# Optimization experiments

Measured on AMD Instinct MI355X. Metric: run time of the kernel, lower is better.

## Reference

```python
import jax, jax.numpy as jnp
import numpy as np

B = 65536
N_SPARSE = 26
N_DENSE = 13
EMB = 5
VOCAB = 100000
N_EXPERTS = 4
D_IN = N_DENSE + N_SPARSE * EMB  # 143
H1, H2 = 128, 64


def setup_inputs() -> dict:
    key = jax.random.key(0)
    ks = jax.random.split(key, 16)
    s = 0.05
    return {
        "sparse_inputs": jax.random.randint(ks[0], (B, N_SPARSE), 0, VOCAB),
        "dense_inputs": jax.random.normal(ks[1], (B, N_DENSE), dtype=jnp.float32),
        "emb_tables": jax.random.normal(ks[2], (N_SPARSE, VOCAB, EMB), dtype=jnp.float32) * s,
        "expert_W1": jax.random.normal(ks[3], (N_EXPERTS, D_IN, H1), dtype=jnp.float32) * s,
        "expert_b1": jnp.zeros((N_EXPERTS, H1), dtype=jnp.float32),
        "expert_W2": jax.random.normal(ks[4], (N_EXPERTS, H1, H2), dtype=jnp.float32) * s,
        "expert_b2": jnp.zeros((N_EXPERTS, H2), dtype=jnp.float32),
        "gate_finish_W": jax.random.normal(ks[5], (D_IN, N_EXPERTS), dtype=jnp.float32) * s,
        "gate_finish_b": jnp.zeros((N_EXPERTS,), dtype=jnp.float32),
        "gate_like_W": jax.random.normal(ks[6], (D_IN, N_EXPERTS), dtype=jnp.float32) * s,
        "gate_like_b": jnp.zeros((N_EXPERTS,), dtype=jnp.float32),
        "finish_W": jax.random.normal(ks[7], (H2, 1), dtype=jnp.float32) * s,
        "finish_b": jnp.zeros((1,), dtype=jnp.float32),
        "like_W": jax.random.normal(ks[8], (H2, 1), dtype=jnp.float32) * s,
        "like_b": jnp.zeros((1,), dtype=jnp.float32),
    }


def reference(sparse_inputs, dense_inputs, emb_tables, expert_W1, expert_b1,
              expert_W2, expert_b2, gate_finish_W, gate_finish_b,
              gate_like_W, gate_like_b, finish_W, finish_b, like_W, like_b):
    # per-feature embedding lookup: [B, N_SPARSE, EMB]
    feat_idx = jnp.arange(N_SPARSE)[None, :]
    sp_emb = emb_tables[feat_idx, sparse_inputs]
    x = jnp.concatenate([dense_inputs, sp_emb.reshape(sparse_inputs.shape[0], -1)], axis=1)  # [B, D_IN]

    # batched expert MLPs (dropout is inactive at inference)
    h = jax.nn.relu(jnp.einsum('bd,edh->beh', x, expert_W1) + expert_b1)  # [B, E, 128]
    expert_out = jax.nn.relu(jnp.einsum('beh,eho->beo', h, expert_W2) + expert_b2)  # [B, E, 64]

    gate_f = jax.nn.softmax(x @ gate_finish_W + gate_finish_b, axis=-1)  # [B, E]
    gate_l = jax.nn.softmax(x @ gate_like_W + gate_like_b, axis=-1)

    task_finish = jnp.einsum('be,beo->bo', gate_f, expert_out)  # [B, 64]
    task_like = jnp.einsum('be,beo->bo', gate_l, expert_out)

    finish = jax.nn.sigmoid(task_finish @ finish_W + finish_b)  # [B, 1]
    like = jax.nn.sigmoid(task_like @ like_W + like_b)  # [B, 1]
    return finish, like
```

## Files before the change

### kernel.cpp

```cpp
#include <hip/hip_runtime.h>
#include <math.h>

#define NB     65536
#define NSP    26
#define NDN    13
#define EMBD   5
#define VOCAB  100000
#define NE     4
#define DIN    143
#define KPAD   160
#define H1     128
#define H2     64

typedef __attribute__((ext_vector_type(8))) short bf16x8;
typedef __attribute__((ext_vector_type(4))) float f32x4;

__device__ __forceinline__ unsigned short f2bf(float f) {
    unsigned int u = __float_as_uint(f);
    u = (u + 0x7fff + ((u >> 16) & 1)) >> 16;
    return (unsigned short)u;
}

__device__ __forceinline__ unsigned cvtpk(float lo, float hi) {
    unsigned r;
    asm("v_cvt_pk_bf16_f32 %0, %1, %2" : "=v"(r) : "v"(lo), "v"(hi));
    return r;
}

__device__ __forceinline__ void gll16(const unsigned short* g, unsigned short* l) {
    __builtin_amdgcn_global_load_lds(
        (const __attribute__((address_space(1))) unsigned int*)g,
        (__attribute__((address_space(3))) unsigned int*)l, 16, 0, 0);
}

#define E1 (4*8*5*512)
#define E2 (4*4*4*512)
#define E3 (5*512)
#define NWE (E1+E2+E3)
#define GBLKS 1024
#define PBLKS ((NWE+255)/256)


__global__ __launch_bounds__(256)
void gather_pack(const int*   __restrict__ sparse,
                 const float* __restrict__ dense,
                 const float* __restrict__ emb,
                 const float* __restrict__ W1,  const float* __restrict__ W2,
                 const float* __restrict__ gfW, const float* __restrict__ glW,
                 unsigned short* __restrict__ w1p, unsigned short* __restrict__ w2p,
                 unsigned short* __restrict__ gwp, unsigned short* __restrict__ xg)
{
    const int blk = blockIdx.x;
    const int tid = threadIdx.x;
    if (blk < GBLKS) {
        __shared__ int idxs[64 * NSP];
        __shared__ __align__(16) unsigned short xs[64][168];
        const int row0 = blk * 64;

        for (int t = tid; t < 64 * NSP; t += 256)
            idxs[t] = sparse[row0 * NSP + t];
        for (int t = tid; t < 64 * NDN; t += 256) {
            int r = t / NDN, c = t - r * NDN;
            xs[r][c] = f2bf(dense[(row0 + r) * NDN + c]);
        }
        for (int t = tid; t < 64 * (KPAD - DIN); t += 256) {
            int r = t / (KPAD - DIN), c = DIN + (t - r * (KPAD - DIN));
            xs[r][c] = 0;
        }
        __syncthreads();
        for (int t = tid; t < 64 * NSP * EMBD; t += 256) {
            int f = t / (64 * EMBD);
            int rem = t - f * (64 * EMBD);
            int r = rem / EMBD, c = rem - r * EMBD;
            int idx = idxs[r * NSP + f];
            float v = emb[((size_t)f * VOCAB + idx) * EMBD + c];
            xs[r][NDN + f * EMBD + c] = f2bf(v);
        }
        __syncthreads();
        for (int v = tid; v < 4 * 5 * 64; v += 256) {
            int lo = v & 63, chunk = v >> 6;
            int s = chunk % 5, tl = chunk / 5;
            int b = lo & 15, g = lo >> 4;
            bf16x8 val = *(const bf16x8*)&xs[tl * 16 + b][32 * s + 8 * g];
            *(bf16x8*)(xg + ((size_t)((blk * 4 + tl) * 5 + s) * 64 + lo) * 8) = val;
        }
        return;
    }

    int i = (blk - GBLKS) * 256 + tid;
    if (i < E1) {
        int j = i & 7, l = (i >> 3) & 63;
        int rest = i >> 9;
        int s = rest % 5; rest /= 5;
        int nt = rest & 7, e = rest >> 3;
        int b = l & 15, g = l >> 4;
        int k = 32 * s + 8 * g + j;
        int n = nt * 16 + b;
        w1p[i] = (k < DIN) ? f2bf(W1[(e * DIN + k) * H1 + n]) : (unsigned short)0;
        return;
    }
    i -= E1;
    if (i < E2) {
        int j = i & 7, l = (i >> 3) & 63;
        int rest = i >> 9;
        int s = rest & 3; rest >>= 2;
        int ot = rest & 3, e = rest >> 2;
        int b = l & 15, g = l >> 4;
        int k = 32 * s + 8 * g + j;
        int o = ot * 16 + b;
        w2p[i] = f2bf(W2[(e * H1 + k) * H2 + o]);
        return;
    }
    i -= E2;
    if (i < E3) {
        int j = i & 7, l = (i >> 3) & 63;
        int s = i >> 9;
        int b = l & 15, g = l >> 4;
        int k = 32 * s + 8 * g + j;
        float v = 0.f;
        if (k < DIN) {
            if (b < 4)      v = gfW[k * NE + b];
            else if (b < 8) v = glW[k * NE + (b - 4)];
        }
        gwp[i] = f2bf(v);
    }
}

__global__ __launch_bounds__(512, 4)
void mmoe10(const unsigned short* __restrict__ xg,
            const unsigned short* __restrict__ w1p, const float* __restrict__ b1,
            const unsigned short* __restrict__ w2p, const float* __restrict__ b2,
            const unsigned short* __restrict__ gwp,
            const float* __restrict__ gfb, const float* __restrict__ glb,
            const float* __restrict__ fW,  const float* __restrict__ lW,
            float* __restrict__ acc)
{
    __shared__ __align__(16) unsigned short wlds[28672];
    __shared__ __align__(16) char hsb[16384];

    const int tid  = threadIdx.x;
    const int wid  = tid >> 6;
    const int lane = tid & 63;
    const int b    = lane & 15;
    const int g    = lane >> 4;
    const int q    = blockIdx.x >> 5;
    const int r5   = blockIdx.x & 31;
    const int e    = r5 >> 3;
    const int rg   = q * 8 + (r5 & 7);
    const int t0   = rg * 8 + wid;
    const int swz  = (b & 7) << 4;
    char* const hw = hsb + wid * 2048 + b * 128;

    #pragma unroll
    for (int i = 0; i < 7; ++i) {
        int c = wid * 7 + i;
        if (c < 40)
            gll16(w1p + (((size_t)e * 40 + c) * 64 + lane) * 8, wlds + c * 512);
        else
            gll16(w2p + (((size_t)e * 16 + (c - 40)) * 64 + lane) * 8,
                  wlds + 20480 + (c - 40) * 512);
    }

    bf16x8 xf[5];
    #pragma unroll
    for (int s = 0; s < 5; ++s)
        xf[s] = *(const bf16x8*)(xg + ((size_t)(t0 * 5 + s) * 64 + lane) * 8);

    f32x4 ga = {0.f, 0.f, 0.f, 0.f};
    #pragma unroll
    for (int s = 0; s < 5; ++s) {
        bf16x8 af = *(const bf16x8*)(gwp + (size_t)(s * 64 + lane) * 8);
        ga = __builtin_amdgcn_mfma_f32_16x16x32_bf16(af, xf[s], ga, 0, 0, 0);
    }
    const float4 gfb4 = *(const float4*)gfb;
    const float4 glb4 = *(const float4*)glb;
    float gfv, glv;
    {
        const float4 bias = (g == 1) ? glb4 : gfb4;
        float l0 = ga[0] + bias.x, l1 = ga[1] + bias.y;
        float l2 = ga[2] + bias.z, l3 = ga[3] + bias.w;
        float m = fmaxf(fmaxf(l0, l1), fmaxf(l2, l3));
        float e0 = expf(l0 - m), e1 = expf(l1 - m), e2 = expf(l2 - m), e3 = expf(l3 - m);
        float inv = 1.f / (e0 + e1 + e2 + e3);
        float sel = (e == 0) ? e0 : (e == 1) ? e1 : (e == 2) ? e2 : e3;
        sel *= inv;
        gfv = __shfl(sel, b);
        glv = __shfl(sel, b + 16);
    }

    __syncthreads();

    f32x4 c[4];
    #pragma unroll
    for (int ot = 0; ot < 4; ++ot) c[ot] = (f32x4){0.f, 0.f, 0.f, 0.f};

    #pragma unroll
    for (int h = 0; h < 2; ++h) {
        #pragma unroll
        for (int nl = 0; nl < 4; ++nl) {
            const int nt = h * 4 + nl;
            bf16x8 wv[5];
            #pragma unroll
            for (int s = 0; s < 5; ++s)
                wv[s] = *(const bf16x8*)(wlds + ((nt * 5 + s) * 64 + lane) * 8);
            f32x4 a2 = {0.f, 0.f, 0.f, 0.f};
            #pragma unroll
            for (int s = 0; s < 5; ++s)
                a2 = __builtin_amdgcn_mfma_f32_16x16x32_bf16(wv[s], xf[s], a2, 0, 0, 0);
            const float4 b1v = *(const float4*)(b1 + e * H1 + nt * 16 + 4 * g);
            uint2 hv;
            hv.x = cvtpk(fmaxf(a2[0] + b1v.x, 0.f), fmaxf(a2[1] + b1v.y, 0.f));
            hv.y = cvtpk(fmaxf(a2[2] + b1v.z, 0.f), fmaxf(a2[3] + b1v.w, 0.f));
            *(uint2*)(hw + ((nl * 32 + g * 8) ^ swz)) = hv;
        }
        bf16x8 hf[2];
        #pragma unroll
        for (int sl = 0; sl < 2; ++sl)
            hf[sl] = *(const bf16x8*)(hw + ((sl * 64 + g * 16) ^ swz));
        #pragma unroll
        for (int ot = 0; ot < 4; ++ot) {
            #pragma unroll
            for (int sl = 0; sl < 2; ++sl) {
                bf16x8 wv2 = *(const bf16x8*)(wlds + 20480 + ((ot * 4 + 2 * h + sl) * 64 + lane) * 8);
                c[ot] = __builtin_amdgcn_mfma_f32_16x16x32_bf16(wv2, hf[sl], c[ot], 0, 0, 0);
            }
        }
    }

    float vf = 0.f, vl = 0.f;
    #pragma unroll
    for (int ot = 0; ot < 4; ++ot) {
        const float4 b2v = *(const float4*)(b2 + e * H2 + ot * 16 + 4 * g);
        const float4 fwv = *(const float4*)(fW + ot * 16 + 4 * g);
        const float4 lwv = *(const float4*)(lW + ot * 16 + 4 * g);
        float o0 = fmaxf(c[ot][0] + b2v.x, 0.f), o1 = fmaxf(c[ot][1] + b2v.y, 0.f);
        float o2 = fmaxf(c[ot][2] + b2v.z, 0.f), o3 = fmaxf(c[ot][3] + b2v.w, 0.f);
        vf += gfv * (o0 * fwv.x + o1 * fwv.y + o2 * fwv.z + o3 * fwv.w);
        vl += glv * (o0 * lwv.x + o1 * lwv.y + o2 * lwv.z + o3 * lwv.w);
    }

    vf += __shfl_xor(vf, 16); vf += __shfl_xor(vf, 32);
    vl += __shfl_xor(vl, 16); vl += __shfl_xor(vl, 32);
    if (g == 0) {
        int r = t0 * 16 + b;
        acc[(size_t)e * NB + r]       = vf;
        acc[(size_t)(4 + e) * NB + r] = vl;
    }
}

__global__ __launch_bounds__(256)
void heads_ep(const float* __restrict__ acc,
              const float* __restrict__ fb, const float* __restrict__ lb,
              float* __restrict__ out)
{
    int r = blockIdx.x * 256 + threadIdx.x;
    float sf = acc[r] + acc[NB + r] + acc[2 * NB + r] + acc[3 * NB + r];
    float sl = acc[4 * NB + r] + acc[5 * NB + r] + acc[6 * NB + r] + acc[7 * NB + r];
    out[r]      = 1.f / (1.f + expf(-(sf + fb[0])));
    out[NB + r] = 1.f / (1.f + expf(-(sl + lb[0])));
}


__global__ __launch_bounds__(256)
void preproc(const float* __restrict__ W1, const float* __restrict__ W2,
             const float* __restrict__ gfW, const float* __restrict__ glW,
             unsigned short* __restrict__ w1t, unsigned short* __restrict__ w2t,
             unsigned short* __restrict__ gwc)
{
    int i = blockIdx.x * 256 + threadIdx.x;
    if (i < 4*128*160) {
        int k = i % KPAD;
        int n = (i / KPAD) & (H1 - 1);
        int e = i / (KPAD * H1);
        w1t[i] = (k < DIN) ? f2bf(W1[(e * DIN + k) * H1 + n]) : (unsigned short)0;
    } else if (i < 4*128*160 + 4*64*128) {
        int j = i - 4*128*160;
        int k = j & (H1 - 1);
        int o = (j >> 7) & (H2 - 1);
        int e = j >> 13;
        w2t[j] = f2bf(W2[(e * H1 + k) * H2 + o]);
    } else if (i < 4*128*160 + 4*64*128 + 16*160) {
        int j = i - (4*128*160 + 4*64*128);
        int k = j % KPAD;
        int r = j / KPAD;
        float v = 0.f;
        if (k < DIN) {
            if (r < 4)      v = gfW[k * NE + r];
            else if (r < 8) v = glW[k * NE + (r - 4)];
        }
        gwc[j] = f2bf(v);
    }
}

__global__ __launch_bounds__(256)
void mmoe_mfma(const int*   __restrict__ sparse,
               const float* __restrict__ dense,
               const float* __restrict__ emb,
               const unsigned short* __restrict__ w1t,
               const float* __restrict__ b1,
               const unsigned short* __restrict__ w2t,
               const float* __restrict__ b2,
               const unsigned short* __restrict__ gwc,
               const float* __restrict__ gfb, const float* __restrict__ glb,
               const float* __restrict__ fW,  const float* __restrict__ fb,
               const float* __restrict__ lW,  const float* __restrict__ lb,
               float* __restrict__ out)
{
    __shared__ __align__(16) unsigned short xs[64][KPAD];
    __shared__ __align__(16) unsigned short hs[64][136];
    __shared__ __align__(16) float gts[64][8];

    const int tid   = threadIdx.x;
    const int wid   = tid >> 6;
    const int lane  = tid & 63;
    const int b     = lane & 15;
    const int g     = lane >> 4;
    const int rbase = wid * 16;
    const int grow0 = blockIdx.x * 64 + rbase;

    for (int t = lane; t < 16 * NDN; t += 64) {
        int r = t & 15, d = t >> 4;
        xs[rbase + r][d] = f2bf(dense[(grow0 + r) * NDN + d]);
    }
    for (int t = lane; t < 16 * (KPAD - DIN); t += 64) {
        int r = t & 15, d = DIN + (t >> 4);
        xs[rbase + r][d] = 0;
    }
    for (int t = lane; t < 16 * NSP; t += 64) {
        int r = t & 15, f = t >> 4;
        int idx = sparse[(grow0 + r) * NSP + f];
        const float* ep = emb + (f * VOCAB + idx) * EMBD;
        int c0 = NDN + EMBD * f;
        #pragma unroll
        for (int c = 0; c < EMBD; ++c)
            xs[rbase + r][c0 + c] = f2bf(ep[c]);
    }

    bf16x8 xf[5];
    #pragma unroll
    for (int s = 0; s < 5; ++s)
        xf[s] = *(const bf16x8*)&xs[rbase + b][32 * s + 8 * g];

    f32x4 ga = {0.f, 0.f, 0.f, 0.f};
    #pragma unroll
    for (int s = 0; s < 5; ++s) {
        bf16x8 af = *(const bf16x8*)(gwc + b * KPAD + 32 * s + 8 * g);
        ga = __builtin_amdgcn_mfma_f32_16x16x32_bf16(af, xf[s], ga, 0, 0, 0);
    }
    if (g < 2) {
        const float4 bias = *(const float4*)(g ? glb : gfb);
        float l0 = ga[0] + bias.x, l1 = ga[1] + bias.y;
        float l2 = ga[2] + bias.z, l3 = ga[3] + bias.w;
        float m = fmaxf(fmaxf(l0, l1), fmaxf(l2, l3));
        float e0 = expf(l0 - m), e1 = expf(l1 - m), e2 = expf(l2 - m), e3 = expf(l3 - m);
        float inv = 1.f / (e0 + e1 + e2 + e3);
        float4 gv; gv.x = e0 * inv; gv.y = e1 * inv; gv.z = e2 * inv; gv.w = e3 * inv;
        *(float4*)&gts[rbase + b][g * 4] = gv;
    }

    float vf = 0.f, vl = 0.f;
    for (int e = 0; e < NE; ++e) {
        const unsigned short* w1e = w1t + e * (H1 * KPAD);
        #pragma unroll
        for (int nt = 0; nt < 8; ++nt) {
            f32x4 acc = {0.f, 0.f, 0.f, 0.f};
            #pragma unroll
            for (int s = 0; s < 5; ++s) {
                bf16x8 af = *(const bf16x8*)(w1e + (nt * 16 + b) * KPAD + 32 * s + 8 * g);
                acc = __builtin_amdgcn_mfma_f32_16x16x32_bf16(af, xf[s], acc, 0, 0, 0);
            }
            const float4 b1v = *(const float4*)(b1 + e * H1 + nt * 16 + 4 * g);
            unsigned lo = (unsigned)f2bf(fmaxf(acc[0] + b1v.x, 0.f)) |
                          ((unsigned)f2bf(fmaxf(acc[1] + b1v.y, 0.f)) << 16);
            unsigned hi = (unsigned)f2bf(fmaxf(acc[2] + b1v.z, 0.f)) |
                          ((unsigned)f2bf(fmaxf(acc[3] + b1v.w, 0.f)) << 16);
            uint2 hv; hv.x = lo; hv.y = hi;
            *(uint2*)&hs[rbase + b][nt * 16 + 4 * g] = hv;
        }

        bf16x8 hf[4];
        #pragma unroll
        for (int s = 0; s < 4; ++s)
            hf[s] = *(const bf16x8*)&hs[rbase + b][32 * s + 8 * g];

        float gf = gts[rbase + b][e];
        float gl = gts[rbase + b][4 + e];
        const unsigned short* w2e = w2t + e * (H2 * H1);
        #pragma unroll
        for (int ot = 0; ot < 4; ++ot) {
            f32x4 acc = {0.f, 0.f, 0.f, 0.f};
            #pragma unroll
            for (int s = 0; s < 4; ++s) {
                bf16x8 af = *(const bf16x8*)(w2e + (ot * 16 + b) * H1 + 32 * s + 8 * g);
                acc = __builtin_amdgcn_mfma_f32_16x16x32_bf16(af, hf[s], acc, 0, 0, 0);
            }
            const float4 b2v = *(const float4*)(b2 + e * H2 + ot * 16 + 4 * g);
            const float4 fwv = *(const float4*)(fW + ot * 16 + 4 * g);
            const float4 lwv = *(const float4*)(lW + ot * 16 + 4 * g);
            float o0 = fmaxf(acc[0] + b2v.x, 0.f);
            float o1 = fmaxf(acc[1] + b2v.y, 0.f);
            float o2 = fmaxf(acc[2] + b2v.z, 0.f);
            float o3 = fmaxf(acc[3] + b2v.w, 0.f);
            vf += gf * (o0 * fwv.x + o1 * fwv.y + o2 * fwv.z + o3 * fwv.w);
            vl += gl * (o0 * lwv.x + o1 * lwv.y + o2 * lwv.z + o3 * lwv.w);
        }
    }

    vf += __shfl_xor(vf, 16); vf += __shfl_xor(vf, 32);
    vl += __shfl_xor(vl, 16); vl += __shfl_xor(vl, 32);
    if (g == 0) {
        int r = grow0 + b;
        out[r]      = 1.f / (1.f + expf(-(vf + fb[0])));
        out[NB + r] = 1.f / (1.f + expf(-(vl + lb[0])));
    }
}


extern "C" void kernel_launch(void* const* d_in, const int* in_sizes, int n_in,
                              void* d_out, int out_size, void* d_ws, size_t ws_size,
                              hipStream_t stream) {
    const int*   sparse = (const int*)  d_in[0];
    const float* dense  = (const float*)d_in[1];
    const float* emb    = (const float*)d_in[2];
    const float* W1     = (const float*)d_in[3];
    const float* b1     = (const float*)d_in[4];
    const float* W2     = (const float*)d_in[5];
    const float* b2     = (const float*)d_in[6];
    const float* gfW    = (const float*)d_in[7];
    const float* gfb    = (const float*)d_in[8];
    const float* glW    = (const float*)d_in[9];
    const float* glb    = (const float*)d_in[10];
    const float* fW     = (const float*)d_in[11];
    const float* fb     = (const float*)d_in[12];
    const float* lW     = (const float*)d_in[13];
    const float* lb     = (const float*)d_in[14];

    const size_t XG_BYTES  = (size_t)NB * KPAD * 2;
    const size_t W_BYTES   = (size_t)NWE * 2;
    const size_t ACC_BYTES = (size_t)2 * 4 * NB * 4;
    const size_t NEED = XG_BYTES + W_BYTES + ACC_BYTES;

    if (ws_size >= NEED) {
        unsigned short* xg  = (unsigned short*)d_ws;
        unsigned short* w1p = (unsigned short*)((char*)d_ws + XG_BYTES);
        unsigned short* w2p = (unsigned short*)((char*)d_ws + XG_BYTES + (size_t)E1 * 2);
        unsigned short* gwp = (unsigned short*)((char*)d_ws + XG_BYTES + (size_t)(E1 + E2) * 2);
        float*          acc = (float*)((char*)d_ws + XG_BYTES + W_BYTES);

        gather_pack<<<GBLKS + PBLKS, 256, 0, stream>>>(
            sparse, dense, emb, W1, W2, gfW, glW, w1p, w2p, gwp, xg);
        mmoe10<<<2048, 512, 0, stream>>>(xg, w1p, b1, w2p, b2, gwp,
                                         gfb, glb, fW, lW, acc);
        heads_ep<<<NB / 256, 256, 0, stream>>>(acc, fb, lb, (float*)d_out);
    } else {
        unsigned short* w1t = (unsigned short*)d_ws;
        unsigned short* w2t = (unsigned short*)((char*)d_ws + 163840);
        unsigned short* gwc = (unsigned short*)((char*)d_ws + 229376);

        int tot = 4*128*160 + 4*64*128 + 16*160;
        preproc<<<(tot + 255) / 256, 256, 0, stream>>>(W1, W2, gfW, glW, w1t, w2t, gwc);
        mmoe_mfma<<<NB / 64, 256, 0, stream>>>(sparse, dense, emb,
                                               w1t, b1, w2t, b2, gwc,
                                               gfb, glb, fW, fb, lW, lb,
                                               (float*)d_out);
    }
}
```

Measured before the change: 63.45 us.

## Fuse gather and heads into single MMoE kernel looping over experts per block

Moves the embedding gather into the main kernel, which builds the bf16 input tile in shared memory instead of reading a staged xg buffer. Each block now loops over all four experts, reloading that expert's packed weights into shared memory each time, and applies the sigmoid heads directly. This removes the xg round trip through global memory, the acc partial-sum buffer and the heads_ep launch. In exchange, weights are reloaded four times per block behind syncthreads with no overlap, and occupancy drops to 256-thread blocks using 64KB of shared memory.

Result: slower. 77.19 us (+21.7%).

```diff
diff --git a/kernel.cpp b/kernel.cpp
--- a/kernel.cpp
+++ b/kernel.cpp
@@ -37,57 +37,16 @@
 #define E2 (4*4*4*512)
 #define E3 (5*512)
 #define NWE (E1+E2+E3)
-#define GBLKS 1024
 #define PBLKS ((NWE+255)/256)
 
 
 __global__ __launch_bounds__(256)
-void gather_pack(const int*   __restrict__ sparse,
-                 const float* __restrict__ dense,
-                 const float* __restrict__ emb,
-                 const float* __restrict__ W1,  const float* __restrict__ W2,
+void weight_pack(const float* __restrict__ W1,  const float* __restrict__ W2,
                  const float* __restrict__ gfW, const float* __restrict__ glW,
                  unsigned short* __restrict__ w1p, unsigned short* __restrict__ w2p,
-                 unsigned short* __restrict__ gwp, unsigned short* __restrict__ xg)
+                 unsigned short* __restrict__ gwp)
 {
-    const int blk = blockIdx.x;
-    const int tid = threadIdx.x;
-    if (blk < GBLKS) {
-        __shared__ int idxs[64 * NSP];
-        __shared__ __align__(16) unsigned short xs[64][168];
-        const int row0 = blk * 64;
-
-        for (int t = tid; t < 64 * NSP; t += 256)
-            idxs[t] = sparse[row0 * NSP + t];
-        for (int t = tid; t < 64 * NDN; t += 256) {
-            int r = t / NDN, c = t - r * NDN;
-            xs[r][c] = f2bf(dense[(row0 + r) * NDN + c]);
-        }
-        for (int t = tid; t < 64 * (KPAD - DIN); t += 256) {
-            int r = t / (KPAD - DIN), c = DIN + (t - r * (KPAD - DIN));
-            xs[r][c] = 0;
-        }
-        __syncthreads();
-        for (int t = tid; t < 64 * NSP * EMBD; t += 256) {
-            int f = t / (64 * EMBD);
-            int rem = t - f * (64 * EMBD);
-            int r = rem / EMBD, c = rem - r * EMBD;
-            int idx = idxs[r * NSP + f];
-            float v = emb[((size_t)f * VOCAB + idx) * EMBD + c];
-            xs[r][NDN + f * EMBD + c] = f2bf(v);
-        }
-        __syncthreads();
-        for (int v = tid; v < 4 * 5 * 64; v += 256) {
-            int lo = v & 63, chunk = v >> 6;
-            int s = chunk % 5, tl = chunk / 5;
-            int b = lo & 15, g = lo >> 4;
-            bf16x8 val = *(const bf16x8*)&xs[tl * 16 + b][32 * s + 8 * g];
-            *(bf16x8*)(xg + ((size_t)((blk * 4 + tl) * 5 + s) * 64 + lo) * 8) = val;
-        }
-        return;
-    }
-
-    int i = (blk - GBLKS) * 256 + tid;
+    int i = blockIdx.x * 256 + threadIdx.x;
     if (i < E1) {
         int j = i & 7, l = (i >> 3) & 63;
         int rest = i >> 9;
@@ -126,45 +85,57 @@
     }
 }
 
-__global__ __launch_bounds__(512, 4)
-void mmoe10(const unsigned short* __restrict__ xg,
+__global__ __launch_bounds__(256, 2)
+void mmoe11(const int*   __restrict__ sparse,
+            const float* __restrict__ dense,
+            const float* __restrict__ emb,
             const unsigned short* __restrict__ w1p, const float* __restrict__ b1,
             const unsigned short* __restrict__ w2p, const float* __restrict__ b2,
             const unsigned short* __restrict__ gwp,
             const float* __restrict__ gfb, const float* __restrict__ glb,
-            const float* __restrict__ fW,  const float* __restrict__ lW,
-            float* __restrict__ acc)
+            const float* __restrict__ fW,  const float* __restrict__ fb,
+            const float* __restrict__ lW,  const float* __restrict__ lb,
+            float* __restrict__ out)
 {
-    __shared__ __align__(16) unsigned short wlds[28672];
-    __shared__ __align__(16) char hsb[16384];
+    __shared__ __align__(16) char uni[65536];
+    unsigned short* const xs   = (unsigned short*)uni;
+    int*            const idxs = (int*)(uni + 21504);
+    unsigned short* const wlds = (unsigned short*)uni;
+    char*           const hsb  = uni + 57344;
 
     const int tid  = threadIdx.x;
     const int wid  = tid >> 6;
     const int lane = tid & 63;
     const int b    = lane & 15;
     const int g    = lane >> 4;
-    const int q    = blockIdx.x >> 5;
-    const int r5   = blockIdx.x & 31;
-    const int e    = r5 >> 3;
-    const int rg   = q * 8 + (r5 & 7);
-    const int t0   = rg * 8 + wid;
+    const int row0 = blockIdx.x * 64;
     const int swz  = (b & 7) << 4;
     char* const hw = hsb + wid * 2048 + b * 128;
 
-    #pragma unroll
-    for (int i = 0; i < 7; ++i) {
-        int c = wid * 7 + i;
-        if (c < 40)
-            gll16(w1p + (((size_t)e * 40 + c) * 64 + lane) * 8, wlds + c * 512);
-        else
-            gll16(w2p + (((size_t)e * 16 + (c - 40)) * 64 + lane) * 8,
-                  wlds + 20480 + (c - 40) * 512);
-    }
+    for (int t = tid; t < 64 * NSP; t += 256)
+        idxs[t] = sparse[row0 * NSP + t];
+    for (int t = tid; t < 64 * NDN; t += 256) {
+        int r = t / NDN, c = t - r * NDN;
+        xs[r * 168 + c] = f2bf(dense[(row0 + r) * NDN + c]);
+    }
+    for (int t = tid; t < 64 * (KPAD - DIN); t += 256) {
+        int r = t / 17, c = DIN + (t - r * 17);
+        xs[r * 168 + c] = 0;
+    }
+    __syncthreads();
+    for (int t = tid; t < 64 * NSP * EMBD; t += 256) {
+        int f = t / 320;
+        int rem = t - f * 320;
+        int r = rem / EMBD, c = rem - r * EMBD;
+        int idx = idxs[r * NSP + f];
+        xs[r * 168 + NDN + f * EMBD + c] = f2bf(emb[((size_t)f * VOCAB + idx) * EMBD + c]);
+    }
+    __syncthreads();
 
     bf16x8 xf[5];
     #pragma unroll
     for (int s = 0; s < 5; ++s)
-        xf[s] = *(const bf16x8*)(xg + ((size_t)(t0 * 5 + s) * 64 + lane) * 8);
+        xf[s] = *(const bf16x8*)&xs[(wid * 16 + b) * 168 + 32 * s + 8 * g];
 
     f32x4 ga = {0.f, 0.f, 0.f, 0.f};
     #pragma unroll
@@ -172,92 +143,93 @@
         bf16x8 af = *(const bf16x8*)(gwp + (size_t)(s * 64 + lane) * 8);
         ga = __builtin_amdgcn_mfma_f32_16x16x32_bf16(af, xf[s], ga, 0, 0, 0);
     }
-    const float4 gfb4 = *(const float4*)gfb;
-    const float4 glb4 = *(const float4*)glb;
-    float gfv, glv;
+    f32x4 gn;
     {
-        const float4 bias = (g == 1) ? glb4 : gfb4;
+        const float4 bias = (g == 1) ? *(const float4*)glb : *(const float4*)gfb;
         float l0 = ga[0] + bias.x, l1 = ga[1] + bias.y;
         float l2 = ga[2] + bias.z, l3 = ga[3] + bias.w;
         float m = fmaxf(fmaxf(l0, l1), fmaxf(l2, l3));
         float e0 = expf(l0 - m), e1 = expf(l1 - m), e2 = expf(l2 - m), e3 = expf(l3 - m);
         float inv = 1.f / (e0 + e1 + e2 + e3);
-        float sel = (e == 0) ? e0 : (e == 1) ? e1 : (e == 2) ? e2 : e3;
-        sel *= inv;
-        gfv = __shfl(sel, b);
-        glv = __shfl(sel, b + 16);
+        gn[0] = e0 * inv; gn[1] = e1 * inv; gn[2] = e2 * inv; gn[3] = e3 * inv;
     }
 
     __syncthreads();
-
-    f32x4 c[4];
-    #pragma unroll
-    for (int ot = 0; ot < 4; ++ot) c[ot] = (f32x4){0.f, 0.f, 0.f, 0.f};
-
-    #pragma unroll
-    for (int h = 0; h < 2; ++h) {
-        #pragma unroll
-        for (int nl = 0; nl < 4; ++nl) {
-            const int nt = h * 4 + nl;
-            bf16x8 wv[5];
-            #pragma unroll
-            for (int s = 0; s < 5; ++s)
-                wv[s] = *(const bf16x8*)(wlds + ((nt * 5 + s) * 64 + lane) * 8);
-            f32x4 a2 = {0.f, 0.f, 0.f, 0.f};
-            #pragma unroll
-            for (int s = 0; s < 5; ++s)
-                a2 = __builtin_amdgcn_mfma_f32_16x16x32_bf16(wv[s], xf[s], a2, 0, 0, 0);
-            const float4 b1v = *(const float4*)(b1 + e * H1 + nt * 16 + 4 * g);
-            uint2 hv;
-            hv.x = cvtpk(fmaxf(a2[0] + b1v.x, 0.f), fmaxf(a2[1] + b1v.y, 0.f));
-            hv.y = cvtpk(fmaxf(a2[2] + b1v.z, 0.f), fmaxf(a2[3] + b1v.w, 0.f));
-            *(uint2*)(hw + ((nl * 32 + g * 8) ^ swz)) = hv;
-        }
-        bf16x8 hf[2];
-        #pragma unroll
-        for (int sl = 0; sl < 2; ++sl)
-            hf[sl] = *(const bf16x8*)(hw + ((sl * 64 + g * 16) ^ swz));
-        #pragma unroll
-        for (int ot = 0; ot < 4; ++ot) {
-            #pragma unroll
-            for (int sl = 0; sl < 2; ++sl) {
-                bf16x8 wv2 = *(const bf16x8*)(wlds + 20480 + ((ot * 4 + 2 * h + sl) * 64 + lane) * 8);
-                c[ot] = __builtin_amdgcn_mfma_f32_16x16x32_bf16(wv2, hf[sl], c[ot], 0, 0, 0);
-            }
-        }
-    }
 
     float vf = 0.f, vl = 0.f;
     #pragma unroll
-    for (int ot = 0; ot < 4; ++ot) {
-        const float4 b2v = *(const float4*)(b2 + e * H2 + ot * 16 + 4 * g);
-        const float4 fwv = *(const float4*)(fW + ot * 16 + 4 * g);
-        const float4 lwv = *(const float4*)(lW + ot * 16 + 4 * g);
-        float o0 = fmaxf(c[ot][0] + b2v.x, 0.f), o1 = fmaxf(c[ot][1] + b2v.y, 0.f);
-        float o2 = fmaxf(c[ot][2] + b2v.z, 0.f), o3 = fmaxf(c[ot][3] + b2v.w, 0.f);
-        vf += gfv * (o0 * fwv.x + o1 * fwv.y + o2 * fwv.z + o3 * fwv.w);
-        vl += glv * (o0 * lwv.x + o1 * lwv.y + o2 * lwv.z + o3 * lwv.w);
+    for (int e = 0; e < NE; ++e) {
+        if (e > 0) __syncthreads();
+        #pragma unroll
+        for (int i = 0; i < 14; ++i) {
+            int c = wid * 14 + i;
+            if (c < 40)
+                gll16(w1p + (((size_t)e * 40 + c) * 64 + lane) * 8, wlds + c * 512);
+            else
+                gll16(w2p + (((size_t)e * 16 + (c - 40)) * 64 + lane) * 8,
+                      wlds + 20480 + (c - 40) * 512);
+        }
+        __syncthreads();
+
+        const float gfv = __shfl(gn[e], b);
+        const float glv = __shfl(gn[e], b + 16);
+
+        f32x4 c4[4];
+        #pragma unroll
+        for (int ot = 0; ot < 4; ++ot) c4[ot] = (f32x4){0.f, 0.f, 0.f, 0.f};
+
+        #pragma unroll
+        for (int h = 0; h < 2; ++h) {
+            #pragma unroll
+            for (int nl = 0; nl < 4; ++nl) {
+                const int nt = h * 4 + nl;
+                bf16x8 wv[5];
+                #pragma unroll
+                for (int s = 0; s < 5; ++s)
+                    wv[s] = *(const bf16x8*)(wlds + ((nt * 5 + s) * 64 + lane) * 8);
+                f32x4 a2 = {0.f, 0.f, 0.f, 0.f};
+                #pragma unroll
+                for (int s = 0; s < 5; ++s)
+                    a2 = __builtin_amdgcn_mfma_f32_16x16x32_bf16(wv[s], xf[s], a2, 0, 0, 0);
+                const float4 b1v = *(const float4*)(b1 + e * H1 + nt * 16 + 4 * g);
+                uint2 hv;
+                hv.x = cvtpk(fmaxf(a2[0] + b1v.x, 0.f), fmaxf(a2[1] + b1v.y, 0.f));
+                hv.y = cvtpk(fmaxf(a2[2] + b1v.z, 0.f), fmaxf(a2[3] + b1v.w, 0.f));
+                *(uint2*)(hw + ((nl * 32 + g * 8) ^ swz)) = hv;
+            }
+            bf16x8 hf[2];
+            #pragma unroll
+            for (int sl = 0; sl < 2; ++sl)
+                hf[sl] = *(const bf16x8*)(hw + ((sl * 64 + g * 16) ^ swz));
+            #pragma unroll
+            for (int ot = 0; ot < 4; ++ot) {
+                #pragma unroll
+                for (int sl = 0; sl < 2; ++sl) {
+                    bf16x8 wv2 = *(const bf16x8*)(wlds + 20480 + ((ot * 4 + 2 * h + sl) * 64 + lane) * 8);
+                    c4[ot] = __builtin_amdgcn_mfma_f32_16x16x32_bf16(wv2, hf[sl], c4[ot], 0, 0, 0);
+                }
+            }
+        }
+
+        #pragma unroll
+        for (int ot = 0; ot < 4; ++ot) {
+            const float4 b2v = *(const float4*)(b2 + e * H2 + ot * 16 + 4 * g);
+            const float4 fwv = *(const float4*)(fW + ot * 16 + 4 * g);
+            const float4 lwv = *(const float4*)(lW + ot * 16 + 4 * g);
+            float o0 = fmaxf(c4[ot][0] + b2v.x, 0.f), o1 = fmaxf(c4[ot][1] + b2v.y, 0.f);
+            float o2 = fmaxf(c4[ot][2] + b2v.z, 0.f), o3 = fmaxf(c4[ot][3] + b2v.w, 0.f);
+            vf += gfv * (o0 * fwv.x + o1 * fwv.y + o2 * fwv.z + o3 * fwv.w);
+            vl += glv * (o0 * lwv.x + o1 * lwv.y + o2 * lwv.z + o3 * lwv.w);
+        }
     }
 
     vf += __shfl_xor(vf, 16); vf += __shfl_xor(vf, 32);
     vl += __shfl_xor(vl, 16); vl += __shfl_xor(vl, 32);
     if (g == 0) {
-        int r = t0 * 16 + b;
-        acc[(size_t)e * NB + r]       = vf;
-        acc[(size_t)(4 + e) * NB + r] = vl;
-    }
-}
-
-__global__ __launch_bounds__(256)
-void heads_ep(const float* __restrict__ acc,
-              const float* __restrict__ fb, const float* __restrict__ lb,
-              float* __restrict__ out)
-{
-    int r = blockIdx.x * 256 + threadIdx.x;
-    float sf = acc[r] + acc[NB + r] + acc[2 * NB + r] + acc[3 * NB + r];
-    float sl = acc[4 * NB + r] + acc[5 * NB + r] + acc[6 * NB + r] + acc[7 * NB + r];
-    out[r]      = 1.f / (1.f + expf(-(sf + fb[0])));
-    out[NB + r] = 1.f / (1.f + expf(-(sl + lb[0])));
+        int r = row0 + wid * 16 + b;
+        out[r]      = 1.f / (1.f + expf(-(vf + fb[0])));
+        out[NB + r] = 1.f / (1.f + expf(-(vl + lb[0])));
+    }
 }
 
 
@@ -435,23 +407,18 @@
     const float* lW     = (const float*)d_in[13];
     const float* lb     = (const float*)d_in[14];
 
-    const size_t XG_BYTES  = (size_t)NB * KPAD * 2;
-    const size_t W_BYTES   = (size_t)NWE * 2;
-    const size_t ACC_BYTES = (size_t)2 * 4 * NB * 4;
-    const size_t NEED = XG_BYTES + W_BYTES + ACC_BYTES;
+    const size_t NEED = (size_t)NWE * 2;
 
     if (ws_size >= NEED) {
-        unsigned short* xg  = (unsigned short*)d_ws;
-        unsigned short* w1p = (unsigned short*)((char*)d_ws + XG_BYTES);
-        unsigned short* w2p = (unsigned short*)((char*)d_ws + XG_BYTES + (size_t)E1 * 2);
-        unsigned short* gwp = (unsigned short*)((char*)d_ws + XG_BYTES + (size_t)(E1 + E2) * 2);
-        float*          acc = (float*)((char*)d_ws + XG_BYTES + W_BYTES);
-
-        gather_pack<<<GBLKS + PBLKS, 256, 0, stream>>>(
-            sparse, dense, emb, W1, W2, gfW, glW, w1p, w2p, gwp, xg);
-        mmoe10<<<2048, 512, 0, stream>>>(xg, w1p, b1, w2p, b2, gwp,
-                                         gfb, glb, fW, lW, acc);
-        heads_ep<<<NB / 256, 256, 0, stream>>>(acc, fb, lb, (float*)d_out);
+        unsigned short* w1p = (unsigned short*)d_ws;
+        unsigned short* w2p = (unsigned short*)((char*)d_ws + (size_t)E1 * 2);
+        unsigned short* gwp = (unsigned short*)((char*)d_ws + (size_t)(E1 + E2) * 2);
+
+        weight_pack<<<PBLKS, 256, 0, stream>>>(W1, W2, gfW, glW, w1p, w2p, gwp);
+        mmoe11<<<NB / 64, 256, 0, stream>>>(sparse, dense, emb,
+                                            w1p, b1, w2p, b2, gwp,
+                                            gfb, glb, fW, fb, lW, lb,
+                                            (float*)d_out);
     } else {
         unsigned short* w1t = (unsigned short*)d_ws;
         unsigned short* w2t = (unsigned short*)((char*)d_ws + 163840);
```
